# Performance work log

Hardware: AMD Instinct MI355X
Metric: run time of the kernel (lower is better)

The kernel has to match this reference:

```python
import jax, jax.numpy as jnp
import numpy as np

T, D_IN, D_OUT, E = 4096, 1024, 4096, 8


def setup_inputs() -> dict:
    key = jax.random.key(0)
    k1, k2, k3 = jax.random.split(key, 3)
    input_tensor = jax.random.normal(k1, (T, D_IN), dtype=jnp.float32)
    # tokens are pre-sorted by expert; contiguous counts per expert (sum == T)
    expert_token_cnt = jnp.full((E,), T // E, dtype=jnp.int32)
    # learned params: nn.init.normal_(mean=0, std=1)
    weight = jax.random.normal(k2, (E, D_OUT, D_IN), dtype=jnp.float32)
    bias = jax.random.normal(k3, (E, D_OUT), dtype=jnp.float32)
    return {"input_tensor": input_tensor, "expert_token_cnt": expert_token_cnt,
            "weight": weight, "bias": bias}


def reference(input_tensor, expert_token_cnt, weight, bias):
    # Grouped GEMM: token t in segment e computes y[t] = x[t] @ W[e].T + b[e]
    # followed by exact (erf) GELU. dropout_rate = 0.0 -> identity.
    n_tok = input_tensor.shape[0]
    n_exp = weight.shape[0]
    bounds = jnp.cumsum(expert_token_cnt)                       # [E]
    expert_id = jnp.searchsorted(bounds, jnp.arange(n_tok), side='right')  # [T]
    onehot = (expert_id[:, None] == jnp.arange(n_exp)[None, :]).astype(input_tensor.dtype)  # [T,E]
    y = jnp.zeros((n_tok, weight.shape[1]), dtype=input_tensor.dtype)
    for e in range(n_exp):  # fixed small expert count; each iter is one masked GEMM
        xe = input_tensor * onehot[:, e][:, None]               # zero out other experts' tokens
        y = y + jnp.einsum('ti,oi->to', xe, weight[e])
    y = y + bias[expert_id]                                     # per-token expert bias
    y = jax.nn.gelu(y, approximate=False)                       # torch default exact GELU
    return y
```

## Files before the change

kernel.cpp:

```cpp
#include <hip/hip_runtime.h>
#include <hip/hip_bf16.h>
#include <math.h>

#define T_TOK 4096
#define DIN   1024
#define DOUT  4096
#define NEXP  8

#define BM 128
#define BN 128
#define BK 64

typedef __bf16 bf16x8 __attribute__((ext_vector_type(8)));
typedef float  f32x4  __attribute__((ext_vector_type(4)));
typedef unsigned short u16x8 __attribute__((ext_vector_type(8)));

__device__ __forceinline__ unsigned short f2bf(float f) {
    union { float f; unsigned u; } x; x.f = f;
    unsigned r = x.u + 0x7FFFu + ((x.u >> 16) & 1u);
    return (unsigned short)(r >> 16);
}

__global__ __launch_bounds__(256) void convert_all(
        const float* __restrict__ srcA, unsigned short* __restrict__ dstA,
        const float* __restrict__ srcW, unsigned short* __restrict__ dstW) {
    const int nA = T_TOK * DIN / 8;
    const int nW = NEXP * DOUT * DIN / 8;
    int i = blockIdx.x * blockDim.x + threadIdx.x;
    const int stride = gridDim.x * blockDim.x;
    for (; i < nA + nW; i += stride) {
        const float* s; unsigned short* d; int idx;
        if (i < nA) { s = srcA; d = dstA; idx = i; }
        else        { s = srcW; d = dstW; idx = i - nA; }
        const f32x4* p = (const f32x4*)(s + (size_t)idx * 8);
        f32x4 v0 = p[0], v1 = p[1];
        u16x8 o;
        #pragma unroll
        for (int q = 0; q < 4; ++q) { o[q] = f2bf(v0[q]); o[4 + q] = f2bf(v1[q]); }
        *(u16x8*)(d + (size_t)idx * 8) = o;
    }
}

__device__ __forceinline__ void gload_lds16(const __bf16* g, __bf16* l) {
    __builtin_amdgcn_global_load_lds(
        (const __attribute__((address_space(1))) unsigned int*)g,
        (__attribute__((address_space(3))) unsigned int*)l,
        16, 0, 0);
}

__global__ __launch_bounds__(256) void moe_gemm(
        const __bf16* __restrict__ A, const __bf16* __restrict__ W,
        const float* __restrict__ bias, const int* __restrict__ cnt,
        float* __restrict__ C) {
    __shared__ __bf16 Asm[BM * BK];
    __shared__ __bf16 Bsm[BN * BK];

    const int tid  = threadIdx.x;
    const int wid  = tid >> 6;
    const int lane = tid & 63;

    const int n_tiles = DOUT / BN;
    const int mt = blockIdx.x / n_tiles;
    const int nt = blockIdx.x % n_tiles;
    const int m0 = mt * BM;
    const int n0 = nt * BN;

    int e = 0, csum = 0;
    #pragma unroll
    for (int i = 0; i < NEXP; ++i) {
        int c = cnt[i];
        if (m0 >= csum + c) { csum += c; e = i + 1; }
    }

    const __bf16* Ab = A + (size_t)m0 * DIN;
    const __bf16* Wb = W + (size_t)e * DOUT * DIN + (size_t)n0 * DIN;

    const int srow = lane >> 3;
    const int sgx  = (lane & 7) ^ srow;

    const int wr_ = wid >> 1, wc_ = wid & 1;
    const int fr  = lane & 15;
    const int fh  = lane >> 4;

    f32x4 acc[4][4];
    #pragma unroll
    for (int i = 0; i < 4; ++i)
        #pragma unroll
        for (int j = 0; j < 4; ++j)
            acc[i][j] = (f32x4)(0.0f);

    for (int kt = 0; kt < DIN; kt += BK) {
        #pragma unroll
        for (int s = 0; s < 4; ++s) {
            const int rbase = wid * 32 + s * 8;
            gload_lds16(Ab + (size_t)(rbase + srow) * DIN + kt + sgx * 8,
                        &Asm[rbase * BK]);
            gload_lds16(Wb + (size_t)(rbase + srow) * DIN + kt + sgx * 8,
                        &Bsm[rbase * BK]);
        }
        __syncthreads();

        #pragma unroll
        for (int ks = 0; ks < 2; ++ks) {
            bf16x8 af[4], bf[4];
            #pragma unroll
            for (int i = 0; i < 4; ++i) {
                const int r = wr_ * 64 + i * 16 + fr;
                const int g = (ks * 4 + fh) ^ (r & 7);
                af[i] = *(const bf16x8*)&Asm[r * BK + g * 8];
            }
            #pragma unroll
            for (int j = 0; j < 4; ++j) {
                const int r = wc_ * 64 + j * 16 + fr;
                const int g = (ks * 4 + fh) ^ (r & 7);
                bf[j] = *(const bf16x8*)&Bsm[r * BK + g * 8];
            }
            #pragma unroll
            for (int i = 0; i < 4; ++i)
                #pragma unroll
                for (int j = 0; j < 4; ++j)
                    acc[i][j] = __builtin_amdgcn_mfma_f32_16x16x32_bf16(
                                    af[i], bf[j], acc[i][j], 0, 0, 0);
        }
        __syncthreads();
    }

    const int colf = lane & 15;
    const int rowf = (lane >> 4) * 4;
    #pragma unroll
    for (int j = 0; j < 4; ++j) {
        const int col = n0 + wc_ * 64 + j * 16 + colf;
        const float bv = bias[(size_t)e * DOUT + col];
        #pragma unroll
        for (int i = 0; i < 4; ++i) {
            #pragma unroll
            for (int r = 0; r < 4; ++r) {
                const int row = m0 + wr_ * 64 + i * 16 + rowf + r;
                float x = acc[i][j][r] + bv;
                float g = 0.5f * x * (1.0f + erff(x * 0.70710678118654752f));
                C[(size_t)row * DOUT + col] = g;
            }
        }
    }
}

extern "C" void kernel_launch(void* const* d_in, const int* in_sizes, int n_in,
                              void* d_out, int out_size, void* d_ws, size_t ws_size,
                              hipStream_t stream) {
    (void)in_sizes; (void)n_in; (void)out_size; (void)ws_size;
    const float* input  = (const float*)d_in[0];
    const int*   cnt    = (const int*)d_in[1];
    const float* weight = (const float*)d_in[2];
    const float* bias   = (const float*)d_in[3];
    float* out = (float*)d_out;

    unsigned short* a_bf = (unsigned short*)d_ws;
    unsigned short* w_bf = a_bf + (size_t)T_TOK * DIN;

    hipLaunchKernelGGL(convert_all, dim3(2048), dim3(256), 0, stream,
                       input, a_bf, weight, w_bf);

    dim3 grid((T_TOK / BM) * (DOUT / BN));
    hipLaunchKernelGGL(moe_gemm, grid, dim3(256), 0, stream,
                       (const __bf16*)a_bf, (const __bf16*)w_bf, bias, cnt, out);
}
```

Baseline: 298.2 us.

## Use 256x256 tiles with 512 threads, double-buffered LDS and block swizzle

Grows the GEMM block tile from 128x128 to 256x256 and runs 8 waves per block, each holding a 128x64 accumulator. LDS is double-buffered so the next K-slice's global-to-LDS loads are issued before computing the current one, cutting to one barrier per iteration. Block IDs are remapped so that neighbouring blocks are spread across M tiles for better L2 reuse of weights. The cost is 128KB of LDS and more registers per block, which limits a CU to one resident block, and exactly 256 blocks may underfill or just fill the device.

```diff
diff --git a/kernel.cpp b/kernel.cpp
--- a/kernel.cpp
+++ b/kernel.cpp
@@ -7,9 +7,10 @@
 #define DOUT  4096
 #define NEXP  8
 
-#define BM 128
-#define BN 128
+#define BM 256
+#define BN 256
 #define BK 64
+#define NT (DIN / BK)
 
 typedef __bf16 bf16x8 __attribute__((ext_vector_type(8)));
 typedef float  f32x4  __attribute__((ext_vector_type(4)));
@@ -48,20 +49,21 @@
         16, 0, 0);
 }
 
-__global__ __launch_bounds__(256) void moe_gemm(
+__global__ __launch_bounds__(512, 2) void moe_gemm(
         const __bf16* __restrict__ A, const __bf16* __restrict__ W,
         const float* __restrict__ bias, const int* __restrict__ cnt,
         float* __restrict__ C) {
-    __shared__ __bf16 Asm[BM * BK];
-    __shared__ __bf16 Bsm[BN * BK];
+    __shared__ __bf16 Asm[2][BM * BK];
+    __shared__ __bf16 Bsm[2][BN * BK];
 
     const int tid  = threadIdx.x;
     const int wid  = tid >> 6;
     const int lane = tid & 63;
 
-    const int n_tiles = DOUT / BN;
-    const int mt = blockIdx.x / n_tiles;
-    const int nt = blockIdx.x % n_tiles;
+    int bid = blockIdx.x;
+    bid = (bid & 7) * 32 + (bid >> 3);
+    const int mt = bid >> 4;
+    const int nt = bid & 15;
     const int m0 = mt * BM;
     const int n0 = nt * BN;
 
@@ -78,64 +80,80 @@
     const int srow = lane >> 3;
     const int sgx  = (lane & 7) ^ srow;
 
-    const int wr_ = wid >> 1, wc_ = wid & 1;
+    const int wr_ = wid >> 2;
+    const int wc_ = wid & 3;
     const int fr  = lane & 15;
     const int fh  = lane >> 4;
 
-    f32x4 acc[4][4];
+    f32x4 acc[8][4];
     #pragma unroll
-    for (int i = 0; i < 4; ++i)
+    for (int i = 0; i < 8; ++i)
         #pragma unroll
         for (int j = 0; j < 4; ++j)
             acc[i][j] = (f32x4)(0.0f);
 
-    for (int kt = 0; kt < DIN; kt += BK) {
+    auto stage = [&](int b, int kt) {
         #pragma unroll
         for (int s = 0; s < 4; ++s) {
             const int rbase = wid * 32 + s * 8;
             gload_lds16(Ab + (size_t)(rbase + srow) * DIN + kt + sgx * 8,
-                        &Asm[rbase * BK]);
+                        &Asm[b][rbase * BK]);
+        }
+        #pragma unroll
+        for (int s = 0; s < 4; ++s) {
+            const int rbase = wid * 32 + s * 8;
             gload_lds16(Wb + (size_t)(rbase + srow) * DIN + kt + sgx * 8,
-                        &Bsm[rbase * BK]);
+                        &Bsm[b][rbase * BK]);
         }
-        __syncthreads();
+    };
 
+    auto compute = [&](int b) {
         #pragma unroll
         for (int ks = 0; ks < 2; ++ks) {
-            bf16x8 af[4], bf[4];
+            bf16x8 af[8], bf[4];
             #pragma unroll
-            for (int i = 0; i < 4; ++i) {
-                const int r = wr_ * 64 + i * 16 + fr;
+            for (int i = 0; i < 8; ++i) {
+                const int r = wr_ * 128 + i * 16 + fr;
                 const int g = (ks * 4 + fh) ^ (r & 7);
-                af[i] = *(const bf16x8*)&Asm[r * BK + g * 8];
+                af[i] = *(const bf16x8*)&Asm[b][r * BK + g * 8];
             }
             #pragma unroll
             for (int j = 0; j < 4; ++j) {
                 const int r = wc_ * 64 + j * 16 + fr;
                 const int g = (ks * 4 + fh) ^ (r & 7);
-                bf[j] = *(const bf16x8*)&Bsm[r * BK + g * 8];
+                bf[j] = *(const bf16x8*)&Bsm[b][r * BK + g * 8];
             }
             #pragma unroll
-            for (int i = 0; i < 4; ++i)
+            for (int i = 0; i < 8; ++i)
                 #pragma unroll
                 for (int j = 0; j < 4; ++j)
                     acc[i][j] = __builtin_amdgcn_mfma_f32_16x16x32_bf16(
                                     af[i], bf[j], acc[i][j], 0, 0, 0);
         }
+    };
+
+    stage(0, 0);
+    __syncthreads();
+    int cur = 0;
+    for (int t = 0; t < NT - 1; ++t) {
+        stage(cur ^ 1, (t + 1) * BK);
+        compute(cur);
         __syncthreads();
+        cur ^= 1;
     }
+    compute(cur);
 
     const int colf = lane & 15;
-    const int rowf = (lane >> 4) * 4;
+    const int rowf = fh * 4;
     #pragma unroll
     for (int j = 0; j < 4; ++j) {
         const int col = n0 + wc_ * 64 + j * 16 + colf;
         const float bv = bias[(size_t)e * DOUT + col];
         #pragma unroll
-        for (int i = 0; i < 4; ++i) {
+        for (int i = 0; i < 8; ++i) {
             #pragma unroll
             for (int r = 0; r < 4; ++r) {
-                const int row = m0 + wr_ * 64 + i * 16 + rowf + r;
+                const int row = m0 + wr_ * 128 + i * 16 + rowf + r;
                 float x = acc[i][j][r] + bv;
                 float g = 0.5f * x * (1.0f + erff(x * 0.70710678118654752f));
                 C[(size_t)row * DOUT + col] = g;
@@ -161,6 +179,6 @@
                        input, a_bf, weight, w_bf);
 
     dim3 grid((T_TOK / BM) * (DOUT / BN));
-    hipLaunchKernelGGL(moe_gemm, grid, dim3(256), 0, stream,
+    hipLaunchKernelGGL(moe_gemm, grid, dim3(512), 0, stream,
                        (const __bf16*)a_bf, (const __bf16*)w_bf, bias, cnt, out);
 }
```

Measured after the change: 292.1 us. 1.02x faster.
